# Optimization experiments

Hardware: AMD Instinct MI355X
Metric: run time of the kernel (lower is better)

The kernel has to match this reference:

```python
import jax, jax.numpy as jnp
import numpy as np

N_NODES = 50000
N_EDGES = 800000
HIDDEN = 128
OUT = 128


def setup_inputs() -> dict:
    key = jax.random.key(0)
    k1, k2, k3, k4, k5, k6 = jax.random.split(key, 6)
    h = jax.random.normal(k1, (N_NODES, HIDDEN), dtype=jnp.float32)
    src = jax.random.randint(k2, (N_EDGES,), 0, N_NODES, dtype=jnp.int64)
    dst = jax.random.randint(k3, (N_EDGES,), 0, N_NODES, dtype=jnp.int64)
    scale = 1.0 / np.sqrt(HIDDEN)
    W_edge = jax.random.normal(k4, (OUT, HIDDEN), dtype=jnp.float32) * scale
    W_self = jax.random.normal(k5, (OUT, HIDDEN), dtype=jnp.float32) * scale
    b_self = jax.random.normal(k6, (OUT,), dtype=jnp.float32) * scale
    return {"h": h, "src": src, "dst": dst, "W_edge": W_edge, "W_self": W_self, "b_self": b_self}


def reference(h, src, dst, W_edge, W_self, b_self):
    n = h.shape[0]
    # edge_transform(src_features): same linear on every edge -> transform nodes once, then gather
    msg_node = h @ W_edge.T                       # [N, OUT]
    msg = msg_node[src]                           # [E, OUT] gather
    sums = jax.ops.segment_sum(msg, dst, num_segments=n)  # [N, OUT] scatter-add
    deg = jax.ops.segment_sum(jnp.ones((dst.shape[0],), dtype=h.dtype), dst, num_segments=n)
    h1 = sums / jnp.maximum(deg, 1.0)[:, None]    # mean; zero in-degree -> 0 (DGL semantics)
    out = jax.nn.relu(h @ W_self.T + b_self + h1)
    return out
```

## Files before the change

kernel.cpp:

```cpp
#include <hip/hip_runtime.h>

#define N_HID 128
#define CAP   32
#define OVF_CAP 8192
#define NSLICE 8
#define PBLK   256

typedef short bf16x8 __attribute__((ext_vector_type(8)));
typedef float f32x4  __attribute__((ext_vector_type(4)));

static __device__ __forceinline__ unsigned short f2bf(float f)
{
    unsigned int u = __float_as_uint(f);
    u = (u + 0x7fffu + ((u >> 16) & 1u)) >> 16;
    return (unsigned short)u;
}
static __device__ __forceinline__ unsigned int pack2(float a, float b)
{
    return (unsigned int)f2bf(a) | ((unsigned int)f2bf(b) << 16);
}
static __device__ __forceinline__ float bf2f(unsigned int bits16)
{
    return __uint_as_float(bits16 << 16);
}
static __device__ __forceinline__ int slice_of(int d, float sln)
{
    int sl = (int)((float)d * sln);
    return sl > NSLICE - 1 ? NSLICE - 1 : sl;
}

__global__ __launch_bounds__(256) void count_fragw_cast(
    const int* __restrict__ dst, int* __restrict__ blockCnt,
    int* __restrict__ cnt, int* __restrict__ ovfn, int E, int n, float sln,
    const float* __restrict__ We, const float* __restrict__ Ws,
    unsigned short* __restrict__ Be, unsigned short* __restrict__ Bs,
    const float* __restrict__ h, unsigned short* __restrict__ hbf, int total)
{
    int t = threadIdx.x, b = blockIdx.x;

    if (b >= PBLK + 16) {
        int idx = (b - PBLK - 16) * 2048 + t * 8;
        if (idx + 8 <= total) {
            float4 v0 = *(const float4*)&h[idx];
            float4 v1 = *(const float4*)&h[idx + 4];
            uint4 pk;
            pk.x = pack2(v0.x, v0.y);
            pk.y = pack2(v0.z, v0.w);
            pk.z = pack2(v1.x, v1.y);
            pk.w = pack2(v1.z, v1.w);
            *(uint4*)&hbf[idx] = pk;
        }
        return;
    }

    if (b >= PBLK) {
        int bb = b - PBLK;
        const float* srcw = (bb < 8) ? We : Ws;
        unsigned short* dstF = (bb < 8) ? Be : Bs;
        int rt = bb & 7;
        int kc = t >> 6, l = t & 63, m = l & 15, q = l >> 4;
        const float* p = &srcw[(size_t)(rt * 16 + m) * N_HID + kc * 32 + q * 8];
        float4 v0 = *(const float4*)p;
        float4 v1 = *(const float4*)(p + 4);
        uint4 pk;
        pk.x = pack2(v0.x, v0.y);
        pk.y = pack2(v0.z, v0.w);
        pk.z = pack2(v1.x, v1.y);
        pk.w = pack2(v1.z, v1.w);
        *(uint4*)&dstF[(size_t)rt * 2048 + kc * 512 + l * 8] = pk;
        return;
    }

    for (int i = b * 256 + t; i < n; i += PBLK * 256) cnt[i] = 0;
    if (b == 0 && t == 0) *ovfn = 0;

    int c[NSLICE];
#pragma unroll
    for (int s = 0; s < NSLICE; ++s) c[s] = 0;

    for (int e = b * 256 + t; e < E; e += PBLK * 256) {
        int sl = slice_of(dst[e], sln);
#pragma unroll
        for (int s = 0; s < NSLICE; ++s) c[s] += (sl == s);
    }

    __shared__ int red[NSLICE * 4];
    int lane = t & 63, wid = t >> 6;
#pragma unroll
    for (int s = 0; s < NSLICE; ++s) {
        int v = c[s];
#pragma unroll
        for (int off = 32; off; off >>= 1) v += __shfl_down(v, off);
        if (lane == 0) red[s * 4 + wid] = v;
    }
    __syncthreads();
    if (t < NSLICE)
        blockCnt[t * PBLK + b] = red[t*4+0] + red[t*4+1] + red[t*4+2] + red[t*4+3];
}

__global__ __launch_bounds__(256) void part_scan(
    const int* __restrict__ blockCnt, int* __restrict__ blockBase,
    int* __restrict__ sbase, int E)
{
    __shared__ int wsm[4];
    int t = threadIdx.x, lane = t & 63, wid = t >> 6;
    int v[8]; int s = 0;
#pragma unroll
    for (int i = 0; i < 8; ++i) { v[i] = blockCnt[t * 8 + i]; s += v[i]; }
    int val = s;
#pragma unroll
    for (int off = 1; off < 64; off <<= 1) {
        int y = __shfl_up(val, off);
        if (lane >= off) val += y;
    }
    if (lane == 63) wsm[wid] = val;
    __syncthreads();
    if (t == 0) { int a = 0; for (int w = 0; w < 4; ++w) { int tmp = wsm[w]; wsm[w] = a; a += tmp; } }
    __syncthreads();
    int excl = wsm[wid] + val - s;
#pragma unroll
    for (int i = 0; i < 8; ++i) { int tv = v[i]; blockBase[t * 8 + i] = excl; excl += tv; }
    __syncthreads();
    if (t < NSLICE) sbase[t] = blockBase[t * PBLK];
    if (t == 0)     sbase[NSLICE] = E;
}

__global__ __launch_bounds__(256) void part_scatter(
    const int* __restrict__ src, const int* __restrict__ dst,
    const int* __restrict__ blockBase, unsigned int* __restrict__ part,
    int E, int n, float sln)
{
    __shared__ int cur[NSLICE];
    int t = threadIdx.x, b = blockIdx.x;
    if (t < NSLICE) cur[t] = blockBase[t * PBLK + b];
    __syncthreads();
    for (int e = b * 256 + t; e < E; e += PBLK * 256) {
        int d = dst[e], s = src[e];
        int sl  = slice_of(d, sln);
        int pos = atomicAdd(&cur[sl], 1);
        part[pos] = ((unsigned int)d << 16) | (unsigned int)s;
    }
}

__global__ __launch_bounds__(256) void bucket_scatter2(
    const unsigned int* __restrict__ part,
    const int* __restrict__ sbase,
    int* __restrict__ cnt,
    unsigned short* __restrict__ bucket,
    int* __restrict__ ovfn,
    long long* __restrict__ ovf)
{
    const int slice = blockIdx.x & 7;
    const int g     = blockIdx.x >> 3;
    const int nG    = (int)(gridDim.x >> 3);
    const int lo    = sbase[slice];
    const int hi    = sbase[slice + 1];
    const int m     = hi - lo;

    const int chunk = (m + nG - 1) / nG;
    const int e0 = lo + g * chunk;
    int e1 = e0 + chunk; if (e1 > hi) e1 = hi;

    for (int e = e0 + (int)threadIdx.x; e < e1; e += 256) {
        unsigned int pk = part[e];
        int d = (int)(pk >> 16);
        int s = (int)(pk & 0xffffu);
        int c = atomicAdd(&cnt[d], 1);
        if (c < CAP) {
            bucket[(size_t)d * CAP + c] = (unsigned short)s;
        } else {
            int o = atomicAdd(ovfn, 1);
            if (o < OVF_CAP) ovf[o] = ((long long)d << 32) | (unsigned int)s;
        }
    }
}

__global__ __launch_bounds__(256) void gather_mean(
    const int* __restrict__ cnt,
    const unsigned short* __restrict__ bucket,
    const int* __restrict__ ovfn,
    const long long* __restrict__ ovf,
    const unsigned short* __restrict__ hbf,
    unsigned short* __restrict__ hagg,
    int n, float sln)
{
    const int slice = blockIdx.x & 7;
    const int g     = blockIdx.x >> 3;
    const int lo    = (int)(((long long)slice * n) / NSLICE);
    const int hi    = (int)(((long long)(slice + 1) * n) / NSLICE);
    int node = lo + g * 4 + ((int)threadIdx.x >> 6);
    if (node >= hi) return;

    int lane = threadIdx.x & 63;
    int deg  = cnt[node];
    int m    = deg < CAP ? deg : CAP;

    const unsigned short* bk = &bucket[(size_t)node * CAP];
    const unsigned int* h32 = (const unsigned int*)hbf;

    float ax = 0.f, ay = 0.f;
    int i = 0;
    for (; i + 4 <= m; i += 4) {
        ushort4 ss = *(const ushort4*)&bk[i];
        unsigned int v0 = h32[(size_t)ss.x * 64 + lane];
        unsigned int v1 = h32[(size_t)ss.y * 64 + lane];
        unsigned int v2 = h32[(size_t)ss.z * 64 + lane];
        unsigned int v3 = h32[(size_t)ss.w * 64 + lane];
        ax += bf2f(v0 & 0xffffu) + bf2f(v1 & 0xffffu) + bf2f(v2 & 0xffffu) + bf2f(v3 & 0xffffu);
        ay += bf2f(v0 >> 16)     + bf2f(v1 >> 16)     + bf2f(v2 >> 16)     + bf2f(v3 >> 16);
    }
    for (; i < m; ++i) {
        unsigned int v = h32[(size_t)bk[i] * 64 + lane];
        ax += bf2f(v & 0xffffu);
        ay += bf2f(v >> 16);
    }

    if (deg > CAP) {
        int no = *ovfn; if (no > OVF_CAP) no = OVF_CAP;
        for (int o = 0; o < no; ++o) {
            long long pk = ovf[o];
            if ((int)(pk >> 32) == node) {
                unsigned int v = h32[(size_t)(unsigned int)pk * 64 + lane];
                ax += bf2f(v & 0xffffu);
                ay += bf2f(v >> 16);
            }
        }
    }

    float sc = deg > 0 ? 1.0f / (float)deg : 0.f;

    int rt = node >> 4, mm = node & 15;
    int kc = lane >> 4, q = (lane >> 2) & 3, j = (lane & 3) * 2;
    unsigned int pk = pack2(ax * sc, ay * sc);
    *(unsigned int*)&hagg[(size_t)rt * 2048 + kc * 512 + (q * 16 + mm) * 8 + j] = pk;
}

__global__ __launch_bounds__(256) void gemm_final(
    const unsigned short* __restrict__ hbf,
    const unsigned short* __restrict__ hagg,
    const unsigned short* __restrict__ Be,
    const unsigned short* __restrict__ Bsf,
    const float* __restrict__ bias,
    float* __restrict__ out,
    int n, int nrt)
{
    int w = (int)((blockIdx.x * blockDim.x + threadIdx.x) >> 6);
    if (w >= nrt) return;
    int l = threadIdx.x & 63;
    int m = l & 15, q = l >> 4;
    int row0 = w * 16;

    bf16x8 ah[4];
#pragma unroll
    for (int kc = 0; kc < 4; ++kc) {
        int gr = row0 + m; if (gr > n - 1) gr = n - 1;
        ah[kc] = *(const bf16x8*)&hbf[(size_t)gr * N_HID + kc * 32 + q * 8];
    }
    const bf16x8* Gp = (const bf16x8*)(hagg + (size_t)w * 2048);
    bf16x8 ag0 = Gp[l], ag1 = Gp[64 + l], ag2 = Gp[128 + l], ag3 = Gp[192 + l];

    const int colb = l & 15;
    const int rq   = (l >> 4) * 4;

#pragma unroll
    for (int ct = 0; ct < 8; ++ct) {
        const bf16x8* BpS = (const bf16x8*)(Bsf + (size_t)ct * 2048);
        const bf16x8* BpE = (const bf16x8*)(Be  + (size_t)ct * 2048);
        f32x4 acc = {0.f, 0.f, 0.f, 0.f};
        acc = __builtin_amdgcn_mfma_f32_16x16x32_bf16(ah[0], BpS[l],       acc, 0, 0, 0);
        acc = __builtin_amdgcn_mfma_f32_16x16x32_bf16(ah[1], BpS[64 + l],  acc, 0, 0, 0);
        acc = __builtin_amdgcn_mfma_f32_16x16x32_bf16(ah[2], BpS[128 + l], acc, 0, 0, 0);
        acc = __builtin_amdgcn_mfma_f32_16x16x32_bf16(ah[3], BpS[192 + l], acc, 0, 0, 0);
        acc = __builtin_amdgcn_mfma_f32_16x16x32_bf16(ag0,   BpE[l],       acc, 0, 0, 0);
        acc = __builtin_amdgcn_mfma_f32_16x16x32_bf16(ag1,   BpE[64 + l],  acc, 0, 0, 0);
        acc = __builtin_amdgcn_mfma_f32_16x16x32_bf16(ag2,   BpE[128 + l], acc, 0, 0, 0);
        acc = __builtin_amdgcn_mfma_f32_16x16x32_bf16(ag3,   BpE[192 + l], acc, 0, 0, 0);

        int col = ct * 16 + colb;
        float bv = bias[col];
#pragma unroll
        for (int r = 0; r < 4; ++r) {
            int row = row0 + rq + r;
            if (row < n) out[(size_t)row * N_HID + col] = fmaxf(acc[r] + bv, 0.f);
        }
    }
}

extern "C" void kernel_launch(void* const* d_in, const int* in_sizes, int n_in,
                              void* d_out, int out_size, void* d_ws, size_t ws_size,
                              hipStream_t stream)
{
    const float* h   = (const float*)d_in[0];
    const int*   src = (const int*)d_in[1];
    const int*   dst = (const int*)d_in[2];
    const float* We  = (const float*)d_in[3];
    const float* Ws  = (const float*)d_in[4];
    const float* bs  = (const float*)d_in[5];
    float*       out = (float*)d_out;

    const int n   = in_sizes[0] / N_HID;
    const int E   = in_sizes[1];
    const int nrt = (n + 15) / 16;
    const float sln = (float)NSLICE / (float)n;
    const int total = n * N_HID;

    unsigned short* hbf  = (unsigned short*)d_ws;
    unsigned short* hagg = hbf + (size_t)n * N_HID;
    unsigned short* bucket = hagg + (size_t)nrt * 2048;
    unsigned short* Be  = bucket + (size_t)n * CAP;
    unsigned short* Bs  = Be + 8 * 2048;
    int*  cnt  = (int*)(Bs + 8 * 2048);
    int*  ovfn = cnt + n;
    long long* ovf = (long long*)(ovfn + 8);
    int*  blockCnt  = (int*)(ovf + OVF_CAP);
    int*  blockBase = blockCnt + PBLK * NSLICE;
    int*  sbase     = blockBase + PBLK * NSLICE;
    unsigned int* part = (unsigned int*)(sbase + 16);

    const int castBlocks = (total + 2047) / 2048;
    const int nodeBlocksPerSlice = ((n / NSLICE) + 4) / 4 + 1;

    count_fragw_cast<<<PBLK + 16 + castBlocks, 256, 0, stream>>>(
        dst, blockCnt, cnt, ovfn, E, n, sln, We, Ws, Be, Bs, h, hbf, total);
    part_scan<<<1, 256, 0, stream>>>(blockCnt, blockBase, sbase, E);
    part_scatter<<<PBLK, 256, 0, stream>>>(src, dst, blockBase, part, E, n, sln);
    bucket_scatter2<<<1024, 256, 0, stream>>>(part, sbase, cnt, bucket, ovfn, ovf);
    gather_mean<<<8 * nodeBlocksPerSlice, 256, 0, stream>>>(cnt, bucket, ovfn, ovf,
                                                            hbf, hagg, n, sln);
    gemm_final<<<(nrt + 3) / 4, 256, 0, stream>>>(hbf, hagg, Be, Bs, bs, out, n, nrt);
}
```

Before: 186.9 us.

## Replace bucket scatter and gather with per-slice LDS atomic aggregation

Edges are now partitioned into 512 destination-node slices instead of 8. Each aggregate block owns one slice of about 100 nodes and accumulates gathered bf16 source features directly into LDS with float atomics, along with per-node degrees. This removes the global per-node bucket array, the global count atomics, the overflow list and one kernel launch. In exchange, LDS atomic contention goes up, the kernel runs only 512 large-LDS blocks, and the single-block prefix scan becomes longer and serial.

```diff
diff --git a/kernel.cpp b/kernel.cpp
--- a/kernel.cpp
+++ b/kernel.cpp
@@ -1,10 +1,9 @@
 #include <hip/hip_runtime.h>
 
 #define N_HID 128
-#define CAP   32
-#define OVF_CAP 8192
-#define NSLICE 8
-#define PBLK   256
+#define NS    512
+#define MAXNS 100
+#define PBLK  128
 
 typedef short bf16x8 __attribute__((ext_vector_type(8)));
 typedef float f32x4  __attribute__((ext_vector_type(4)));
@@ -23,15 +22,13 @@
 {
     return __uint_as_float(bits16 << 16);
 }
-static __device__ __forceinline__ int slice_of(int d, float sln)
-{
-    int sl = (int)((float)d * sln);
-    return sl > NSLICE - 1 ? NSLICE - 1 : sl;
+static __device__ __forceinline__ int slice_of(int d, int n)
+{
+    return (d * NS) / n;
 }
 
 __global__ __launch_bounds__(256) void count_fragw_cast(
-    const int* __restrict__ dst, int* __restrict__ blockCnt,
-    int* __restrict__ cnt, int* __restrict__ ovfn, int E, int n, float sln,
+    const int* __restrict__ dst, int* __restrict__ blockCnt, int E, int n,
     const float* __restrict__ We, const float* __restrict__ Ws,
     unsigned short* __restrict__ Be, unsigned short* __restrict__ Bs,
     const float* __restrict__ h, unsigned short* __restrict__ hbf, int total)
@@ -71,31 +68,14 @@
         return;
     }
 
-    for (int i = b * 256 + t; i < n; i += PBLK * 256) cnt[i] = 0;
-    if (b == 0 && t == 0) *ovfn = 0;
-
-    int c[NSLICE];
-#pragma unroll
-    for (int s = 0; s < NSLICE; ++s) c[s] = 0;
-
-    for (int e = b * 256 + t; e < E; e += PBLK * 256) {
-        int sl = slice_of(dst[e], sln);
-#pragma unroll
-        for (int s = 0; s < NSLICE; ++s) c[s] += (sl == s);
-    }
-
-    __shared__ int red[NSLICE * 4];
-    int lane = t & 63, wid = t >> 6;
-#pragma unroll
-    for (int s = 0; s < NSLICE; ++s) {
-        int v = c[s];
-#pragma unroll
-        for (int off = 32; off; off >>= 1) v += __shfl_down(v, off);
-        if (lane == 0) red[s * 4 + wid] = v;
-    }
-    __syncthreads();
-    if (t < NSLICE)
-        blockCnt[t * PBLK + b] = red[t*4+0] + red[t*4+1] + red[t*4+2] + red[t*4+3];
+    __shared__ int hist[NS];
+    hist[t] = 0; hist[t + 256] = 0;
+    __syncthreads();
+    for (int e = b * 256 + t; e < E; e += PBLK * 256)
+        atomicAdd(&hist[slice_of(dst[e], n)], 1);
+    __syncthreads();
+    blockCnt[t * PBLK + b]         = hist[t];
+    blockCnt[(t + 256) * PBLK + b] = hist[t + 256];
 }
 
 __global__ __launch_bounds__(256) void part_scan(
@@ -104,9 +84,9 @@
 {
     __shared__ int wsm[4];
     int t = threadIdx.x, lane = t & 63, wid = t >> 6;
-    int v[8]; int s = 0;
-#pragma unroll
-    for (int i = 0; i < 8; ++i) { v[i] = blockCnt[t * 8 + i]; s += v[i]; }
+    int base = t * 256;
+    int s = 0;
+    for (int i = 0; i < 256; ++i) s += blockCnt[base + i];
     int val = s;
 #pragma unroll
     for (int off = 1; off < 64; off <<= 1) {
@@ -118,121 +98,103 @@
     if (t == 0) { int a = 0; for (int w = 0; w < 4; ++w) { int tmp = wsm[w]; wsm[w] = a; a += tmp; } }
     __syncthreads();
     int excl = wsm[wid] + val - s;
-#pragma unroll
-    for (int i = 0; i < 8; ++i) { int tv = v[i]; blockBase[t * 8 + i] = excl; excl += tv; }
-    __syncthreads();
-    if (t < NSLICE) sbase[t] = blockBase[t * PBLK];
-    if (t == 0)     sbase[NSLICE] = E;
+    for (int i = 0; i < 256; ++i) {
+        int v = blockCnt[base + i];
+        blockBase[base + i] = excl;
+        excl += v;
+    }
+    __syncthreads();
+    sbase[t]       = blockBase[t * PBLK];
+    sbase[t + 256] = blockBase[(t + 256) * PBLK];
+    if (t == 0) sbase[NS] = E;
 }
 
 __global__ __launch_bounds__(256) void part_scatter(
     const int* __restrict__ src, const int* __restrict__ dst,
     const int* __restrict__ blockBase, unsigned int* __restrict__ part,
-    int E, int n, float sln)
-{
-    __shared__ int cur[NSLICE];
+    int E, int n)
+{
+    __shared__ int cur[NS];
     int t = threadIdx.x, b = blockIdx.x;
-    if (t < NSLICE) cur[t] = blockBase[t * PBLK + b];
+    cur[t]       = blockBase[t * PBLK + b];
+    cur[t + 256] = blockBase[(t + 256) * PBLK + b];
     __syncthreads();
     for (int e = b * 256 + t; e < E; e += PBLK * 256) {
         int d = dst[e], s = src[e];
-        int sl  = slice_of(d, sln);
+        int sl  = slice_of(d, n);
         int pos = atomicAdd(&cur[sl], 1);
         part[pos] = ((unsigned int)d << 16) | (unsigned int)s;
     }
 }
 
-__global__ __launch_bounds__(256) void bucket_scatter2(
+__global__ __launch_bounds__(256) void aggregate(
     const unsigned int* __restrict__ part,
     const int* __restrict__ sbase,
-    int* __restrict__ cnt,
-    unsigned short* __restrict__ bucket,
-    int* __restrict__ ovfn,
-    long long* __restrict__ ovf)
-{
-    const int slice = blockIdx.x & 7;
-    const int g     = blockIdx.x >> 3;
-    const int nG    = (int)(gridDim.x >> 3);
-    const int lo    = sbase[slice];
-    const int hi    = sbase[slice + 1];
-    const int m     = hi - lo;
-
-    const int chunk = (m + nG - 1) / nG;
-    const int e0 = lo + g * chunk;
-    int e1 = e0 + chunk; if (e1 > hi) e1 = hi;
-
-    for (int e = e0 + (int)threadIdx.x; e < e1; e += 256) {
-        unsigned int pk = part[e];
-        int d = (int)(pk >> 16);
-        int s = (int)(pk & 0xffffu);
-        int c = atomicAdd(&cnt[d], 1);
-        if (c < CAP) {
-            bucket[(size_t)d * CAP + c] = (unsigned short)s;
-        } else {
-            int o = atomicAdd(ovfn, 1);
-            if (o < OVF_CAP) ovf[o] = ((long long)d << 32) | (unsigned int)s;
-        }
-    }
-}
-
-__global__ __launch_bounds__(256) void gather_mean(
-    const int* __restrict__ cnt,
-    const unsigned short* __restrict__ bucket,
-    const int* __restrict__ ovfn,
-    const long long* __restrict__ ovf,
     const unsigned short* __restrict__ hbf,
     unsigned short* __restrict__ hagg,
-    int n, float sln)
-{
-    const int slice = blockIdx.x & 7;
-    const int g     = blockIdx.x >> 3;
-    const int lo    = (int)(((long long)slice * n) / NSLICE);
-    const int hi    = (int)(((long long)(slice + 1) * n) / NSLICE);
-    int node = lo + g * 4 + ((int)threadIdx.x >> 6);
-    if (node >= hi) return;
-
-    int lane = threadIdx.x & 63;
-    int deg  = cnt[node];
-    int m    = deg < CAP ? deg : CAP;
-
-    const unsigned short* bk = &bucket[(size_t)node * CAP];
+    int n)
+{
+    __shared__ float acc[MAXNS * N_HID];
+    __shared__ int   degs[MAXNS];
+
+    int t = threadIdx.x;
+    int s = blockIdx.x;
+    int lo_node = (s * n + NS - 1) / NS;
+    int hi_node = ((s + 1) * n + NS - 1) / NS;
+    int ns = hi_node - lo_node;
+
+    for (int i = t; i < MAXNS * N_HID; i += 256) acc[i] = 0.f;
+    for (int i = t; i < MAXNS; i += 256) degs[i] = 0;
+    __syncthreads();
+
+    int lane = t & 63, w = t >> 6;
+    int e0 = sbase[s], e1 = sbase[s + 1];
+    int nEdges = e1 - e0;
     const unsigned int* h32 = (const unsigned int*)hbf;
 
-    float ax = 0.f, ay = 0.f;
-    int i = 0;
-    for (; i + 4 <= m; i += 4) {
-        ushort4 ss = *(const ushort4*)&bk[i];
-        unsigned int v0 = h32[(size_t)ss.x * 64 + lane];
-        unsigned int v1 = h32[(size_t)ss.y * 64 + lane];
-        unsigned int v2 = h32[(size_t)ss.z * 64 + lane];
-        unsigned int v3 = h32[(size_t)ss.w * 64 + lane];
-        ax += bf2f(v0 & 0xffffu) + bf2f(v1 & 0xffffu) + bf2f(v2 & 0xffffu) + bf2f(v3 & 0xffffu);
-        ay += bf2f(v0 >> 16)     + bf2f(v1 >> 16)     + bf2f(v2 >> 16)     + bf2f(v3 >> 16);
-    }
-    for (; i < m; ++i) {
-        unsigned int v = h32[(size_t)bk[i] * 64 + lane];
-        ax += bf2f(v & 0xffffu);
-        ay += bf2f(v >> 16);
-    }
-
-    if (deg > CAP) {
-        int no = *ovfn; if (no > OVF_CAP) no = OVF_CAP;
-        for (int o = 0; o < no; ++o) {
-            long long pk = ovf[o];
-            if ((int)(pk >> 32) == node) {
-                unsigned int v = h32[(size_t)(unsigned int)pk * 64 + lane];
-                ax += bf2f(v & 0xffffu);
-                ay += bf2f(v >> 16);
+    for (int c0 = w * 64; c0 < nEdges; c0 += 256) {
+        int rem = nEdges - c0;
+        int nv  = rem < 64 ? rem : 64;
+        unsigned int pk = (lane < nv) ? part[e0 + c0 + lane] : 0u;
+
+        int j = 0;
+        for (; j + 8 <= nv; j += 8) {
+            unsigned int vv[8]; int dl[8];
+#pragma unroll
+            for (int k = 0; k < 8; ++k) {
+                unsigned int pkj = __shfl(pk, j + k);
+                dl[k] = (int)(pkj >> 16) - lo_node;
+                vv[k] = h32[(size_t)(pkj & 0xffffu) * 64 + lane];
             }
-        }
-    }
-
-    float sc = deg > 0 ? 1.0f / (float)deg : 0.f;
-
-    int rt = node >> 4, mm = node & 15;
-    int kc = lane >> 4, q = (lane >> 2) & 3, j = (lane & 3) * 2;
-    unsigned int pk = pack2(ax * sc, ay * sc);
-    *(unsigned int*)&hagg[(size_t)rt * 2048 + kc * 512 + (q * 16 + mm) * 8 + j] = pk;
+#pragma unroll
+            for (int k = 0; k < 8; ++k) {
+                atomicAdd(&acc[dl[k] * N_HID + 2 * lane],     bf2f(vv[k] & 0xffffu));
+                atomicAdd(&acc[dl[k] * N_HID + 2 * lane + 1], bf2f(vv[k] >> 16));
+                if (lane == 0) atomicAdd(&degs[dl[k]], 1);
+            }
+        }
+        for (; j < nv; ++j) {
+            unsigned int pkj = __shfl(pk, j);
+            int dl = (int)(pkj >> 16) - lo_node;
+            unsigned int v = h32[(size_t)(pkj & 0xffffu) * 64 + lane];
+            atomicAdd(&acc[dl * N_HID + 2 * lane],     bf2f(v & 0xffffu));
+            atomicAdd(&acc[dl * N_HID + 2 * lane + 1], bf2f(v >> 16));
+            if (lane == 0) atomicAdd(&degs[dl], 1);
+        }
+    }
+    __syncthreads();
+
+    for (int i = w; i < ns; i += 4) {
+        int dg = degs[i];
+        float sc = dg > 0 ? 1.0f / (float)dg : 0.f;
+        float a0 = acc[i * N_HID + 2 * lane] * sc;
+        float a1 = acc[i * N_HID + 2 * lane + 1] * sc;
+        int node = lo_node + i;
+        int rt = node >> 4, mm = node & 15;
+        int kc = lane >> 4, q = (lane >> 2) & 3, jj = (lane & 3) * 2;
+        *(unsigned int*)&hagg[(size_t)rt * 2048 + kc * 512 + (q * 16 + mm) * 8 + jj]
+            = pack2(a0, a1);
+    }
 }
 
 __global__ __launch_bounds__(256) void gemm_final(
@@ -301,31 +263,23 @@
     const int n   = in_sizes[0] / N_HID;
     const int E   = in_sizes[1];
     const int nrt = (n + 15) / 16;
-    const float sln = (float)NSLICE / (float)n;
     const int total = n * N_HID;
 
     unsigned short* hbf  = (unsigned short*)d_ws;
     unsigned short* hagg = hbf + (size_t)n * N_HID;
-    unsigned short* bucket = hagg + (size_t)nrt * 2048;
-    unsigned short* Be  = bucket + (size_t)n * CAP;
-    unsigned short* Bs  = Be + 8 * 2048;
-    int*  cnt  = (int*)(Bs + 8 * 2048);
-    int*  ovfn = cnt + n;
-    long long* ovf = (long long*)(ovfn + 8);
-    int*  blockCnt  = (int*)(ovf + OVF_CAP);
-    int*  blockBase = blockCnt + PBLK * NSLICE;
-    int*  sbase     = blockBase + PBLK * NSLICE;
-    unsigned int* part = (unsigned int*)(sbase + 16);
+    unsigned short* Be   = hagg + (size_t)nrt * 2048;
+    unsigned short* Bs   = Be + 8 * 2048;
+    int* blockCnt  = (int*)(Bs + 8 * 2048);
+    int* blockBase = blockCnt + NS * PBLK;
+    int* sbase     = blockBase + NS * PBLK;
+    unsigned int* part = (unsigned int*)(sbase + NS + 16);
 
     const int castBlocks = (total + 2047) / 2048;
-    const int nodeBlocksPerSlice = ((n / NSLICE) + 4) / 4 + 1;
 
     count_fragw_cast<<<PBLK + 16 + castBlocks, 256, 0, stream>>>(
-        dst, blockCnt, cnt, ovfn, E, n, sln, We, Ws, Be, Bs, h, hbf, total);
+        dst, blockCnt, E, n, We, Ws, Be, Bs, h, hbf, total);
     part_scan<<<1, 256, 0, stream>>>(blockCnt, blockBase, sbase, E);
-    part_scatter<<<PBLK, 256, 0, stream>>>(src, dst, blockBase, part, E, n, sln);
-    bucket_scatter2<<<1024, 256, 0, stream>>>(part, sbase, cnt, bucket, ovfn, ovf);
-    gather_mean<<<8 * nodeBlocksPerSlice, 256, 0, stream>>>(cnt, bucket, ovfn, ovf,
-                                                            hbf, hagg, n, sln);
+    part_scatter<<<PBLK, 256, 0, stream>>>(src, dst, blockBase, part, E, n);
+    aggregate<<<NS, 256, 0, stream>>>(part, sbase, hbf, hagg, n);
     gemm_final<<<(nrt + 3) / 4, 256, 0, stream>>>(hbf, hagg, Be, Bs, bs, out, n, nrt);
 }
```

New measurement: 699.6 us. 274% more time.
